# Optimization experiments

Hardware: AMD Instinct MI355X
Metric: run time of the kernel (lower is better)

## Reference

```python
import jax, jax.numpy as jnp
import numpy as np

# Constants from the module's docstrings / vm_step / constants
VOCAB = 272
D_MODEL = 512
CODE_START = 256  # Token.CODE_START (first special after 256 byte tokens)
CODE_END = 257    # Token.CODE_END
MEM = 258         # Token.MEM
ADDR_KEY = 206    # _SetDim.ADDR_KEY (48 dims: 3 nibbles x 16 one-hot)
MEM_STORE = 455   # _SetDim.MEM_STORE
BYTES_PER_INSTR = 5
INSTR_WIDTH = 8


def setup_inputs() -> dict:
    key = jax.random.key(0)
    k1, k2 = jax.random.split(key)
    token_ids = jax.random.randint(k1, (32, 8192), 0, VOCAB)
    embed_table = jax.random.normal(k2, (VOCAB, D_MODEL), dtype=jnp.float32)
    return {"token_ids": token_ids, "embed_table": embed_table, "mem_history_end": 2048}


def reference(token_ids, embed_table, mem_history_end):
    B, S = token_ids.shape
    x = embed_table[token_ids]                     # [B, S, D] gather
    pos = jnp.arange(S)

    # ---- ADDR_KEY injection (vectorized replacement of the per-token loop) ----
    is_cs = token_ids == CODE_START
    is_ce = token_ids == CODE_END
    # most recent CODE_START position at or before i (-1 if none yet)
    cs = jax.lax.cummax(jnp.where(is_cs, pos[None, :], -1), axis=1)       # [B, S]
    # the python loop breaks the row at the FIRST CODE_END
    first_ce = jnp.min(jnp.where(is_ce, pos[None, :], S), axis=1, keepdims=True)  # [B, 1]
    is_byte = token_ids < 256
    mask = (cs >= 0) & (pos[None, :] < first_ce) & is_byte                # [B, S]

    seq_pos = jnp.maximum(pos[None, :] - cs - 1, 0)                       # >=0 where mask
    addr = (seq_pos // BYTES_PER_INSTR) * INSTR_WIDTH + seq_pos % BYTES_PER_INSTR
    lo = addr & 15
    hi = (addr >> 4) & 15
    top = (addr >> 8) & 15

    nib = jnp.arange(16)
    onehot48 = jnp.concatenate(
        [lo[..., None] == nib, hi[..., None] == nib, top[..., None] == nib], axis=-1
    )  # [B, S, 48] bool

    seg = x[..., ADDR_KEY:ADDR_KEY + 48]
    seg = jnp.where(mask[..., None] & onehot48, jnp.float32(1.0), seg)
    x = x.at[..., ADDR_KEY:ADDR_KEY + 48].set(seg)

    # ---- MEM_STORE injection on historical MEM markers ----
    mem_mask = (token_ids == MEM) & (pos[None, :] < mem_history_end)
    ch = jnp.where(mem_mask, jnp.float32(1.0), x[..., MEM_STORE])
    x = x.at[..., MEM_STORE].set(ch)
    return x
```

## Files before the change

### kernel.cpp

```cpp
#include <hip/hip_runtime.h>
#include <hip/hip_bf16.h>

#define B 32
#define S 8192
#define D 512
#define CODE_START 256
#define CODE_END 257
#define MEM_TOK 258
#define ADDR_KEY 206
#define MEM_STORE 455
#define SUB 128
#define NSUB (S / SUB)

typedef float f32x4 __attribute__((ext_vector_type(4)));
typedef int i32x4 __attribute__((ext_vector_type(4)));

__device__ inline int make_pack(int tk, int cs, int p, int f, int mhe) {
  int pk = tk;
  if ((cs >= 0) && (p < f) && (tk < 256)) {
    int sp = p - cs - 1;
    if (sp < 0) sp = 0;
    int q = sp / 5;
    int r = sp - q * 5;
    int addr = q * 8 + r;
    pk |= (1 << 9) | ((addr & 15) << 12) | (((addr >> 4) & 15) << 16) |
          (((addr >> 8) & 15) << 20);
  }
  if (tk == MEM_TOK && p < mhe) pk |= (1 << 10);
  return pk;
}

__global__ __launch_bounds__(256) void nvm_fused(
    const int* __restrict__ tok, const float* __restrict__ table,
    const int* __restrict__ mhe_p, float* __restrict__ out) {
  const int c = blockIdx.x;
  const int b = blockIdx.y;
  const int tid = threadIdx.x;
  const int lane = tid & 63, wid = tid >> 6;
  const int base = c * SUB;
  const int* row = tok + b * S;

  __shared__ int red_max[4], red_min[4], wt[2];
  __shared__ int pack_sh[SUB];

  int vmax = -1, vmin = S;
  #pragma unroll
  for (int k = 0; k < 8; ++k) {
    const i32x4 q = reinterpret_cast<const i32x4*>(row)[tid + 256 * k];
    const int p = 4 * (tid + 256 * k);
    #pragma unroll
    for (int e = 0; e < 4; ++e) {
      const int t = q[e], pp = p + e;
      if (t == CODE_START && pp < base) vmax = max(vmax, pp);
      if (t == CODE_END) vmin = min(vmin, pp);
    }
  }
  #pragma unroll
  for (int off = 32; off; off >>= 1) {
    vmax = max(vmax, __shfl_down(vmax, off, 64));
    vmin = min(vmin, __shfl_down(vmin, off, 64));
  }
  if (lane == 0) { red_max[wid] = vmax; red_min[wid] = vmin; }

  int myTok = 0, v = -1;
  if (tid < SUB) {
    myTok = row[base + tid];
    v = (myTok == CODE_START) ? (base + tid) : -1;
  }
  int incl = v;
  #pragma unroll
  for (int off = 1; off < 64; off <<= 1) {
    const int u = __shfl_up(incl, off, 64);
    if (lane >= off) incl = max(incl, u);
  }
  if (tid < SUB && lane == 63) wt[wid] = incl;
  __syncthreads();

  const int pre = max(max(red_max[0], red_max[1]), max(red_max[2], red_max[3]));
  const int fce = min(min(red_min[0], red_min[1]), min(red_min[2], red_min[3]));
  const int mhe = mhe_p[0];

  if (tid < SUB) {
    const int ex = (wid == 1) ? wt[0] : -1;
    const int cs = max(max(incl, ex), pre);
    pack_sh[tid] = make_pack(myTok, cs, base + tid, fce, mhe);
  }
  __syncthreads();

  const int ln = tid & 127, half = tid >> 7;
  const int c0 = ln * 4;
  float* outb = out + (size_t)(b * S + base) * D;

  #pragma unroll 4
  for (int j = 0; j < SUB / 2; ++j) {
    const int i = 2 * j + half;
    const int p = pack_sh[i];
    const int tk = p & 511;
    f32x4 v4 = *reinterpret_cast<const f32x4*>(table + tk * D + c0);
    if (p & (1 << 9)) {
      const int ca = ADDR_KEY + ((p >> 12) & 15);
      const int cb = ADDR_KEY + 16 + ((p >> 16) & 15);
      const int cc = ADDR_KEY + 32 + ((p >> 20) & 15);
      #pragma unroll
      for (int u = 0; u < 4; ++u) {
        const int ch = c0 + u;
        if (ch == ca || ch == cb || ch == cc) v4[u] = 1.0f;
      }
    }
    if ((p & (1 << 10)) && c0 == (MEM_STORE & ~3)) v4[MEM_STORE & 3] = 1.0f;
    __builtin_nontemporal_store(v4, reinterpret_cast<f32x4*>(outb + (size_t)i * D + c0));
  }
}

extern "C" void kernel_launch(void* const* d_in, const int* in_sizes, int n_in,
                              void* d_out, int out_size, void* d_ws, size_t ws_size,
                              hipStream_t stream) {
  const int* tok = (const int*)d_in[0];
  const float* table = (const float*)d_in[1];
  const int* mhe = (const int*)d_in[2];
  float* out = (float*)d_out;

  nvm_fused<<<dim3(NSUB, B), 256, 0, stream>>>(tok, table, mhe, out);
}
```

Before: 106.4 us.

## Split into token-pack prepass and persistent grid-stride gather kernel

Splits the fused kernel in two. The first kernel computes packed per-token metadata (CODE_START scan, first CODE_END, MEM flag) over 512-token chunks and writes it to workspace. The second is a fixed-size grid-stride kernel that gathers embedding rows and applies the overrides. This cuts the redundant full-row reductions, which previously ran once per 128-token block, and decouples the store-bound gather from the scan. The cost is a second launch and a round trip of the pack array through global memory.

```diff
diff --git a/kernel.cpp b/kernel.cpp
--- a/kernel.cpp
+++ b/kernel.cpp
@@ -9,8 +9,8 @@
 #define MEM_TOK 258
 #define ADDR_KEY 206
 #define MEM_STORE 455
-#define SUB 128
-#define NSUB (S / SUB)
+#define CHUNK 512
+#define NCH (S / CHUNK)
 
 typedef float f32x4 __attribute__((ext_vector_type(4)));
 typedef int i32x4 __attribute__((ext_vector_type(4)));
@@ -30,18 +30,31 @@
   return pk;
 }
 
-__global__ __launch_bounds__(256) void nvm_fused(
-    const int* __restrict__ tok, const float* __restrict__ table,
-    const int* __restrict__ mhe_p, float* __restrict__ out) {
-  const int c = blockIdx.x;
-  const int b = blockIdx.y;
+__global__ __launch_bounds__(256) void nvm_pack(
+    const int* __restrict__ tok, const int* __restrict__ mhe_p,
+    int* __restrict__ pack) {
+  const int c = blockIdx.x, b = blockIdx.y;
   const int tid = threadIdx.x;
   const int lane = tid & 63, wid = tid >> 6;
-  const int base = c * SUB;
+  const int base = c * CHUNK;
   const int* row = tok + b * S;
 
-  __shared__ int red_max[4], red_min[4], wt[2];
-  __shared__ int pack_sh[SUB];
+  __shared__ int red_max[4], red_min[4], wt[4];
+
+  const int s0 = base + 2 * tid, s1 = s0 + 1;
+  const int2 tt = reinterpret_cast<const int2*>(row + base)[tid];
+  const int v0 = (tt.x == CODE_START) ? s0 : -1;
+  const int v1 = (tt.y == CODE_START) ? s1 : -1;
+  const int i1 = max(v0, v1);
+  int incl = i1;
+  #pragma unroll
+  for (int off = 1; off < 64; off <<= 1) {
+    const int u = __shfl_up(incl, off, 64);
+    if (lane >= off) incl = max(incl, u);
+  }
+  int ex = __shfl_up(incl, 1, 64);
+  if (lane == 0) ex = -1;
+  if (lane == 63) wt[wid] = incl;
 
   int vmax = -1, vmin = S;
   #pragma unroll
@@ -61,42 +74,34 @@
     vmin = min(vmin, __shfl_down(vmin, off, 64));
   }
   if (lane == 0) { red_max[wid] = vmax; red_min[wid] = vmin; }
-
-  int myTok = 0, v = -1;
-  if (tid < SUB) {
-    myTok = row[base + tid];
-    v = (myTok == CODE_START) ? (base + tid) : -1;
-  }
-  int incl = v;
-  #pragma unroll
-  for (int off = 1; off < 64; off <<= 1) {
-    const int u = __shfl_up(incl, off, 64);
-    if (lane >= off) incl = max(incl, u);
-  }
-  if (tid < SUB && lane == 63) wt[wid] = incl;
   __syncthreads();
 
-  const int pre = max(max(red_max[0], red_max[1]), max(red_max[2], red_max[3]));
+  int pre = max(max(red_max[0], red_max[1]), max(red_max[2], red_max[3]));
+  for (int w = 0; w < wid; ++w) pre = max(pre, wt[w]);
   const int fce = min(min(red_min[0], red_min[1]), min(red_min[2], red_min[3]));
   const int mhe = mhe_p[0];
 
-  if (tid < SUB) {
-    const int ex = (wid == 1) ? wt[0] : -1;
-    const int cs = max(max(incl, ex), pre);
-    pack_sh[tid] = make_pack(myTok, cs, base + tid, fce, mhe);
-  }
-  __syncthreads();
+  ex = max(ex, pre);
+  const int cs0 = max(ex, v0);
+  const int cs1 = max(ex, i1);
 
-  const int ln = tid & 127, half = tid >> 7;
-  const int c0 = ln * 4;
-  float* outb = out + (size_t)(b * S + base) * D;
+  pack[b * S + s0] = make_pack(tt.x, cs0, s0, fce, mhe);
+  pack[b * S + s1] = make_pack(tt.y, cs1, s1, fce, mhe);
+}
 
-  #pragma unroll 4
-  for (int j = 0; j < SUB / 2; ++j) {
-    const int i = 2 * j + half;
-    const int p = pack_sh[i];
+__global__ __launch_bounds__(256) void nvm_main(
+    const int* __restrict__ pack, const float* __restrict__ table,
+    float* __restrict__ out) {
+  const int lane = threadIdx.x & 127;
+  const int half = threadIdx.x >> 7;
+  const int c0 = lane * 4;
+  const int NTP = B * S / 2;
+
+  for (int tp = blockIdx.x; tp < NTP; tp += gridDim.x) {
+    const int t = tp * 2 + half;
+    const int p = pack[t];
     const int tk = p & 511;
-    f32x4 v4 = *reinterpret_cast<const f32x4*>(table + tk * D + c0);
+    f32x4 v = *reinterpret_cast<const f32x4*>(table + tk * D + c0);
     if (p & (1 << 9)) {
       const int ca = ADDR_KEY + ((p >> 12) & 15);
       const int cb = ADDR_KEY + 16 + ((p >> 16) & 15);
@@ -104,11 +109,11 @@
       #pragma unroll
       for (int u = 0; u < 4; ++u) {
         const int ch = c0 + u;
-        if (ch == ca || ch == cb || ch == cc) v4[u] = 1.0f;
+        if (ch == ca || ch == cb || ch == cc) v[u] = 1.0f;
       }
     }
-    if ((p & (1 << 10)) && c0 == (MEM_STORE & ~3)) v4[MEM_STORE & 3] = 1.0f;
-    __builtin_nontemporal_store(v4, reinterpret_cast<f32x4*>(outb + (size_t)i * D + c0));
+    if ((p & (1 << 10)) && c0 == (MEM_STORE & ~3)) v[MEM_STORE & 3] = 1.0f;
+    __builtin_nontemporal_store(v, reinterpret_cast<f32x4*>(out + (size_t)t * D + c0));
   }
 }
 
@@ -120,5 +125,8 @@
   const int* mhe = (const int*)d_in[2];
   float* out = (float*)d_out;
 
-  nvm_fused<<<dim3(NSUB, B), 256, 0, stream>>>(tok, table, mhe, out);
+  int* pack = (int*)d_ws;
+
+  nvm_pack<<<dim3(NCH, B), 256, 0, stream>>>(tok, mhe, pack);
+  nvm_main<<<4096, 256, 0, stream>>>(pack, table, out);
 }
```

Result: faster. 100.8 us (-5.3%).
